# Optimization experiments

Hardware: AMD Instinct MI355X
Metric: run time of the kernel (lower is better)

The kernel has to match this reference:

```python
import jax, jax.numpy as jnp
import numpy as np

NUM_HEAD = 8
HEAD_DIM = 64
TEMPERATURE = 10000.0


def positional_encoding(L, D):
    # Mirrors get_positional_encoding: sin on even-indexed, cos on odd-indexed
    # columns of pos, interleaved via stack+reshape.
    embed = jnp.arange(L, dtype=jnp.float32)
    dim_t = jnp.arange(D, dtype=jnp.float32)
    dim_t = TEMPERATURE ** (2.0 * jnp.floor(dim_t / 2.0) / D)
    pos = embed[:, None] / dim_t                      # [L, D]
    pos = jnp.stack([jnp.sin(pos[:, 0::2]), jnp.cos(pos[:, 1::2])], axis=2)
    return pos.reshape(1, L, D)                       # [1, L, D]


def setup_inputs() -> dict:
    key = jax.random.key(0)
    ks = jax.random.split(key, 4)
    B, L, D = 8, 1024, 256
    HD = NUM_HEAD * HEAD_DIM                          # 512
    glorot = float(np.sqrt(2.0 / (D + HD)))
    return {
        "x": jax.random.normal(ks[0], (B, L, D), jnp.float32),
        "Wq": jax.random.normal(ks[1], (D, HD), jnp.float32) * glorot,
        "bq": jnp.zeros((NUM_HEAD,), jnp.float32),
        "Wk": jax.random.normal(ks[2], (D, HD), jnp.float32) * glorot,
        "bk": jnp.zeros((NUM_HEAD,), jnp.float32),
        "Wv": jax.random.normal(ks[3], (D, HD), jnp.float32) * glorot,
        "bv": jnp.zeros((NUM_HEAD,), jnp.float32),
    }


def reference(x, Wq, bq, Wk, bk, Wv, bv):
    B, L, D = x.shape
    pe = positional_encoding(L, D)
    qk_in = x + pe                                    # query/key get pos-enc, value does not
    # per-head bias broadcast over head_dim (tf.repeat(bias, head_dim))
    q = qk_in @ Wq + jnp.repeat(bq, HEAD_DIM)
    k = qk_in @ Wk + jnp.repeat(bk, HEAD_DIM)
    v = x @ Wv + jnp.repeat(bv, HEAD_DIM)
    split = lambda t: t.reshape(B, L, NUM_HEAD, HEAD_DIM)
    q, k, v = split(q), split(k), split(v)
    att = jnp.einsum('blhd,bmhd->bhlm', q, k) * (float(HEAD_DIM) ** -0.5)
    att = jax.nn.softmax(att, axis=-1)                # [B, H, L, L]
    out = jnp.einsum('bhlm,bmhd->blhd', att, v)       # [B, L, H, hd]
    return out.reshape(B, L, NUM_HEAD * HEAD_DIM)
```

## Files before the change

### kernel.cpp

```cpp
#include <hip/hip_runtime.h>
#include <hip/hip_bf16.h>

#define NB   8
#define NL   1024
#define ND   256
#define NH   8
#define NHD  64
#define NC   512
#define NTOK (NB*NL)

typedef __bf16 bf16x8v __attribute__((ext_vector_type(8)));
typedef float f32x4 __attribute__((ext_vector_type(4)));

__device__ __forceinline__ unsigned short f2bf(float f) {
  unsigned u = __float_as_uint(f);
  unsigned r = (u + 0x7fffu + ((u >> 16) & 1u)) >> 16;
  return (unsigned short)r;
}

__device__ __forceinline__ unsigned pack_bf16x2(float lo, float hi) {
  __hip_bfloat162 h2 = __float22bfloat162_rn(make_float2(lo, hi));
  union { __hip_bfloat162 h; unsigned u; } cvt;
  cvt.h = h2;
  return cvt.u;
}

__global__ __launch_bounds__(256) void gemm_qkv_fused_kernel(
    const float* __restrict__ x,
    const float* __restrict__ Wq, const float* __restrict__ Wk,
    const float* __restrict__ Wv,
    const float* __restrict__ bq, const float* __restrict__ bk,
    const float* __restrict__ bv,
    unsigned short* __restrict__ qg, unsigned short* __restrict__ kg,
    unsigned short* __restrict__ vg) {
  __shared__ unsigned short As[128 * 72];
  __shared__ unsigned short Bs[128 * 72];

  const int z = blockIdx.z;
  const float* Wsrc = (z == 0) ? Wq : (z == 1) ? Wk : Wv;
  const float* bias = (z == 0) ? bq : (z == 1) ? bk : bv;
  unsigned short* Out = (z == 0) ? qg : (z == 1) ? kg : vg;
  const float scale = (z == 0) ? 0.18033688011112042f : 1.0f;
  const bool addpe = (z < 2);

  const int nt = blockIdx.x;
  const int mt = blockIdx.y;
  const int tid = threadIdx.x;
  const int w = tid >> 6;
  const int wm = w >> 1, wn = w & 1;
  const int lane = tid & 63;
  const int lg = lane >> 4, lr = lane & 15;

  const int r0 = tid >> 3, c8 = tid & 7;
  unsigned short* Adst = As + r0 * 72 + 8 * ((c8 + 2 * (r0 & 7)) & 7);
  const float* xbase = x + (size_t)(mt * 128 + r0) * ND + c8 * 8;
  const int no = tid & 15, kp0 = tid >> 4;

  f32x4 acc[4][4] = {};

  for (int kb = 0; kb < 4; ++kb) {
    if (kb) __syncthreads();
    float i0 = 0.f, i1 = 0.f, i2 = 0.f, i3 = 0.f;
    if (addpe) {
      int dh = kb * 32 + c8 * 4;
      i0 = __expf(-0.07195578415606394f * (float)(dh));
      i1 = __expf(-0.07195578415606394f * (float)(dh + 1));
      i2 = __expf(-0.07195578415606394f * (float)(dh + 2));
      i3 = __expf(-0.07195578415606394f * (float)(dh + 3));
    }
#pragma unroll
    for (int i = 0; i < 4; ++i) {
      int row = r0 + 32 * i;
      f32x4 xa = *(const f32x4*)(xbase + (size_t)(32 * i) * ND + kb * 64);
      f32x4 xc = *(const f32x4*)(xbase + (size_t)(32 * i) * ND + kb * 64 + 4);
      unsigned p0, p1, p2, p3;
      if (addpe) {
        float l = (float)((mt * 128 + row) & (NL - 1));
        float a0 = l * i0, a1 = l * i1, a2 = l * i2, a3 = l * i3;
        p0 = pack_bf16x2(xa[0] + __sinf(a0), xa[1] + __cosf(a0));
        p1 = pack_bf16x2(xa[2] + __sinf(a1), xa[3] + __cosf(a1));
        p2 = pack_bf16x2(xc[0] + __sinf(a2), xc[1] + __cosf(a2));
        p3 = pack_bf16x2(xc[2] + __sinf(a3), xc[3] + __cosf(a3));
      } else {
        p0 = pack_bf16x2(xa[0], xa[1]);
        p1 = pack_bf16x2(xa[2], xa[3]);
        p2 = pack_bf16x2(xc[0], xc[1]);
        p3 = pack_bf16x2(xc[2], xc[3]);
      }
      int4 pv; pv.x = (int)p0; pv.y = (int)p1; pv.z = (int)p2; pv.w = (int)p3;
      *(int4*)(Adst + (size_t)(32 * i) * 72) = pv;
    }
#pragma unroll
    for (int u = 0; u < 2; ++u) {
      int kp = kp0 + 16 * u;
      int krow = kb * 64 + 2 * kp;
      const float* wr0 = Wsrc + (size_t)krow * NC + nt * 128 + no * 8;
      const float* wr1 = wr0 + NC;
      f32x4 w0a = *(const f32x4*)(wr0);
      f32x4 w0b = *(const f32x4*)(wr0 + 4);
      f32x4 w1a = *(const f32x4*)(wr1);
      f32x4 w1b = *(const f32x4*)(wr1 + 4);
#pragma unroll
      for (int e = 0; e < 8; ++e) {
        float lo = (e < 4) ? w0a[e] : w0b[e - 4];
        float hi = (e < 4) ? w1a[e] : w1b[e - 4];
        int n = no * 8 + e;
        *(unsigned*)(Bs + n * 72 + 8 * (((kp >> 2) + (no & 7)) & 7) +
                     (kp & 3) * 2) = pack_bf16x2(lo, hi);
      }
    }
    __syncthreads();

#pragma unroll
    for (int kk = 0; kk < 2; ++kk) {
      bf16x8v a[4], b[4];
#pragma unroll
      for (int mi = 0; mi < 4; ++mi) {
        int row = wm * 64 + mi * 16 + lr;
        a[mi] = *(const bf16x8v*)(As + row * 72 +
                                  8 * ((4 * kk + lg + 2 * (row & 7)) & 7));
      }
#pragma unroll
      for (int nj = 0; nj < 4; ++nj) {
        int n = wn * 64 + nj * 16 + lr;
        b[nj] = *(const bf16x8v*)(Bs + n * 72 +
                                  8 * ((4 * kk + lg + ((n >> 3) & 7)) & 7));
      }
#pragma unroll
      for (int mi = 0; mi < 4; ++mi)
#pragma unroll
        for (int nj = 0; nj < 4; ++nj)
          acc[mi][nj] = __builtin_amdgcn_mfma_f32_16x16x32_bf16(
              a[mi], b[nj], acc[mi][nj], 0, 0, 0);
    }
  }

  const float bval = bias[nt * 2 + wn];
  const int h = nt * 2 + wn;
#pragma unroll
  for (int mi = 0; mi < 4; ++mi) {
#pragma unroll
    for (int nj = 0; nj < 4; ++nj) {
#pragma unroll
      for (int j = 0; j < 4; ++j) {
        int r = mt * 128 + wm * 64 + mi * 16 + lg * 4 + j;
        int dd = nj * 16 + lr;
        int bb = r >> 10, lpos = r & (NL - 1);
        float val = (acc[mi][nj][j] + bval) * scale;
        if (z < 2)
          Out[((bb * NH + h) * NL + lpos) * NHD + dd] = f2bf(val);
        else
          Out[((bb * NH + h) * NHD + dd) * NL + lpos] = f2bf(val);
      }
    }
  }
}

__global__ __launch_bounds__(256) void attn_kernel(
    const unsigned short* __restrict__ Q,
    const unsigned short* __restrict__ K,
    const unsigned short* __restrict__ Vt,
    float* __restrict__ Out) {
  __shared__ unsigned short Ks[64 * 72];
  __shared__ unsigned short Vs[64 * 72];
  __shared__ unsigned short Ps[64 * 72];

  const int qt = blockIdx.x;
  const int bh = blockIdx.y;
  const int bb = bh >> 3, h = bh & 7;
  const int tid = threadIdx.x;
  const int w = tid >> 6;
  const int lane = tid & 63;
  const int lg = lane >> 4, lr = lane & 15;
  const int qrow0 = qt * 64 + w * 16;

  bf16x8v qf[2];
#pragma unroll
  for (int kk = 0; kk < 2; ++kk)
    qf[kk] = *(const bf16x8v*)(Q + ((size_t)bh * NL + qrow0 + lr) * NHD + kk * 32 + lg * 8);

  const int r0 = tid >> 3;
  const int c8 = tid & 7;
  const unsigned short* kp0 = K + (size_t)bh * NL * NHD + r0 * NHD + c8 * 8;
  const unsigned short* vp0 = Vt + ((size_t)bh * NHD + r0) * NL + c8 * 8;
  const int sw_st = 8 * ((c8 + 2 * (r0 & 7)) & 7);
  unsigned short* kdst = Ks + r0 * 72 + sw_st;
  unsigned short* vdst = Vs + r0 * 72 + sw_st;

  float m_ = -1e30f, lsum = 0.0f;
  f32x4 o[4] = {};
  int4 ka, kc, va, vc;

#define KVLOADS(kv)                                             \
  ka = *(const int4*)(kp0 + (kv) * 64 * NHD);                   \
  kc = *(const int4*)(kp0 + (kv) * 64 * NHD + 32 * NHD);        \
  va = *(const int4*)(vp0 + (kv) * 64);                         \
  vc = *(const int4*)(vp0 + (kv) * 64 + 32 * NL);

  KVLOADS(0)
  for (int kv = 0; kv < 16; ++kv) {
    if (kv) __syncthreads();
    *(int4*)(kdst)           = ka;
    *(int4*)(kdst + 32 * 72) = kc;
    *(int4*)(vdst)           = va;
    *(int4*)(vdst + 32 * 72) = vc;
    if (kv < 15) { KVLOADS(kv + 1) }
    __syncthreads();

    f32x4 s[4] = {};
    __builtin_amdgcn_s_setprio(1);
#pragma unroll
    for (int kk = 0; kk < 2; ++kk) {
#pragma unroll
      for (int nb = 0; nb < 4; ++nb) {
        int row = nb * 16 + lr;
        bf16x8v kf = *(const bf16x8v*)(Ks + row * 72 +
                                       8 * ((4 * kk + lg + 2 * (row & 7)) & 7));
        s[nb] = __builtin_amdgcn_mfma_f32_16x16x32_bf16(kf, qf[kk], s[nb], 0, 0, 0);
      }
    }
    __builtin_amdgcn_s_setprio(0);

    float tm;
    {
      float a0 = fmaxf(s[0][0], s[0][1]), a1 = fmaxf(s[0][2], s[0][3]);
      float a2 = fmaxf(s[1][0], s[1][1]), a3 = fmaxf(s[1][2], s[1][3]);
      float a4 = fmaxf(s[2][0], s[2][1]), a5 = fmaxf(s[2][2], s[2][3]);
      float a6 = fmaxf(s[3][0], s[3][1]), a7 = fmaxf(s[3][2], s[3][3]);
      float c0 = fmaxf(fmaxf(a0, a1), fmaxf(a2, a3));
      float c1 = fmaxf(fmaxf(a4, a5), fmaxf(a6, a7));
      tm = fmaxf(c0, c1);
    }
    tm = fmaxf(tm, __shfl_xor(tm, 16, 64));
    tm = fmaxf(tm, __shfl_xor(tm, 32, 64));
    if (__any(tm > m_ + 8.0f)) {
      float nm = fmaxf(m_, tm);
      float corr = exp2f(m_ - nm);
      m_ = nm;
      lsum *= corr;
#pragma unroll
      for (int db = 0; db < 4; ++db)
#pragma unroll
        for (int j = 0; j < 4; ++j) o[db][j] *= corr;
    }
#pragma unroll
    for (int nb = 0; nb < 4; ++nb)
#pragma unroll
      for (int j = 0; j < 4; ++j)
        s[nb][j] = exp2f(s[nb][j] - m_);
    float ts;
    {
      float a0 = s[0][0] + s[0][1], a1 = s[0][2] + s[0][3];
      float a2 = s[1][0] + s[1][1], a3 = s[1][2] + s[1][3];
      float a4 = s[2][0] + s[2][1], a5 = s[2][2] + s[2][3];
      float a6 = s[3][0] + s[3][1], a7 = s[3][2] + s[3][3];
      ts = ((a0 + a1) + (a2 + a3)) + ((a4 + a5) + (a6 + a7));
    }
    ts += __shfl_xor(ts, 16, 64);
    ts += __shfl_xor(ts, 32, 64);
    lsum += ts;

    {
      int prow = w * 16 + lr;
      unsigned short* pbase = Ps + prow * 72;
      int key = 2 * (lr & 7);
#pragma unroll
      for (int nb = 0; nb < 4; ++nb)
#pragma unroll
        for (int hh = 0; hh < 2; ++hh) {
          int slot = 2 * nb + (lg >> 1);
          *(unsigned*)(pbase + 8 * ((slot + key) & 7) + (lg & 1) * 4 + 2 * hh) =
              pack_bf16x2(s[nb][2 * hh], s[nb][2 * hh + 1]);
        }
    }

    __builtin_amdgcn_s_setprio(1);
#pragma unroll
    for (int kk = 0; kk < 2; ++kk) {
      int prow = w * 16 + lr;
      bf16x8v pf = *(const bf16x8v*)(Ps + prow * 72 +
                                     8 * ((4 * kk + lg + 2 * (lr & 7)) & 7));
#pragma unroll
      for (int db = 0; db < 4; ++db) {
        int row = db * 16 + lr;
        bf16x8v vf = *(const bf16x8v*)(Vs + row * 72 +
                                       8 * ((4 * kk + lg + 2 * (row & 7)) & 7));
        o[db] = __builtin_amdgcn_mfma_f32_16x16x32_bf16(vf, pf, o[db], 0, 0, 0);
      }
    }
    __builtin_amdgcn_s_setprio(0);
  }
#undef KVLOADS

  float inv = 1.0f / lsum;
  int q = qrow0 + lr;
#pragma unroll
  for (int db = 0; db < 4; ++db) {
    f32x4 ov;
#pragma unroll
    for (int j = 0; j < 4; ++j) ov[j] = o[db][j] * inv;
    *(f32x4*)(Out + (size_t)(bb * NL + q) * NC + h * NHD + db * 16 + lg * 4) = ov;
  }
}

extern "C" void kernel_launch(void* const* d_in, const int* in_sizes, int n_in,
                              void* d_out, int out_size, void* d_ws, size_t ws_size,
                              hipStream_t stream) {
  const float* x  = (const float*)d_in[0];
  const float* Wq = (const float*)d_in[1];
  const float* bq = (const float*)d_in[2];
  const float* Wk = (const float*)d_in[3];
  const float* bk = (const float*)d_in[4];
  const float* Wv = (const float*)d_in[5];
  const float* bv = (const float*)d_in[6];
  float* out = (float*)d_out;

  unsigned short* qg = (unsigned short*)d_ws;
  unsigned short* kg = qg + (size_t)NB * NH * NL * NHD;
  unsigned short* vg = kg + (size_t)NB * NH * NL * NHD;

  gemm_qkv_fused_kernel<<<dim3(4, 64, 3), 256, 0, stream>>>(
      x, Wq, Wk, Wv, bq, bk, bv, qg, kg, vg);

  attn_kernel<<<dim3(16, 64), 256, 0, stream>>>(qg, kg, vg, out);
}
```

Baseline: 134.5 us.

## Stage V transpose through LDS and drop XOR swizzle in attention tiles

For the V projection, the GEMM epilogue now writes the tile transposed into shared memory and then stores 128-bit contiguous rows to the transposed V output. Before, each thread issued strided 2-byte scattered stores. The attention kernel removes the XOR swizzle on the K, V and P shared tiles and relies on the 72-element row padding alone to avoid bank conflicts, which simplifies address arithmetic. The tradeoff is two extra barriers in the V epilogue and possibly more LDS bank conflicts in attention without the swizzle.

```diff
diff --git a/kernel.cpp b/kernel.cpp
--- a/kernel.cpp
+++ b/kernel.cpp
@@ -33,8 +33,9 @@
     const float* __restrict__ bv,
     unsigned short* __restrict__ qg, unsigned short* __restrict__ kg,
     unsigned short* __restrict__ vg) {
-  __shared__ unsigned short As[128 * 72];
-  __shared__ unsigned short Bs[128 * 72];
+  __shared__ unsigned short smem[2 * 128 * 72];
+  unsigned short* As = smem;
+  unsigned short* Bs = smem + 128 * 72;
 
   const int z = blockIdx.z;
   const float* Wsrc = (z == 0) ? Wq : (z == 1) ? Wk : Wv;
@@ -137,22 +138,48 @@
 
   const float bval = bias[nt * 2 + wn];
   const int h = nt * 2 + wn;
-#pragma unroll
-  for (int mi = 0; mi < 4; ++mi) {
-#pragma unroll
-    for (int nj = 0; nj < 4; ++nj) {
-#pragma unroll
-      for (int j = 0; j < 4; ++j) {
-        int r = mt * 128 + wm * 64 + mi * 16 + lg * 4 + j;
-        int dd = nj * 16 + lr;
-        int bb = r >> 10, lpos = r & (NL - 1);
-        float val = (acc[mi][nj][j] + bval) * scale;
-        if (z < 2)
+  if (z < 2) {
+#pragma unroll
+    for (int mi = 0; mi < 4; ++mi) {
+#pragma unroll
+      for (int nj = 0; nj < 4; ++nj) {
+#pragma unroll
+        for (int j = 0; j < 4; ++j) {
+          int r = mt * 128 + wm * 64 + mi * 16 + lg * 4 + j;
+          int dd = nj * 16 + lr;
+          int bb = r >> 10, lpos = r & (NL - 1);
+          float val = (acc[mi][nj][j] + bval) * scale;
           Out[((bb * NH + h) * NL + lpos) * NHD + dd] = f2bf(val);
-        else
-          Out[((bb * NH + h) * NHD + dd) * NL + lpos] = f2bf(val);
-      }
-    }
+        }
+      }
+    }
+  } else {
+    __syncthreads();
+    unsigned short* Ts = smem;
+#pragma unroll
+    for (int mi = 0; mi < 4; ++mi)
+#pragma unroll
+      for (int nj = 0; nj < 4; ++nj)
+#pragma unroll
+        for (int jp = 0; jp < 2; ++jp) {
+          int c = wn * 64 + nj * 16 + lr;
+          int r = wm * 64 + mi * 16 + lg * 4 + jp * 2;
+          *(unsigned*)(Ts + c * 136 + r) =
+              pack_bf16x2(acc[mi][nj][jp * 2] + bval,
+                          acc[mi][nj][jp * 2 + 1] + bval);
+        }
+    __syncthreads();
+    int row = tid >> 1, half = tid & 1;
+    int hh = nt * 2 + (row >> 6);
+    int ddl = row & 63;
+    int bb2 = (mt * 128) >> 10;
+    int lpos0 = (mt * 128) & (NL - 1);
+    unsigned short* dst =
+        Out + ((size_t)(bb2 * NH + hh) * NHD + ddl) * NL + lpos0 + half * 64;
+    const unsigned short* src = Ts + row * 136 + half * 64;
+#pragma unroll
+    for (int i = 0; i < 8; ++i)
+      *(int4*)(dst + i * 8) = *(const int4*)(src + i * 8);
   }
 }
 
@@ -180,12 +207,11 @@
     qf[kk] = *(const bf16x8v*)(Q + ((size_t)bh * NL + qrow0 + lr) * NHD + kk * 32 + lg * 8);
 
   const int r0 = tid >> 3;
-  const int c8 = tid & 7;
-  const unsigned short* kp0 = K + (size_t)bh * NL * NHD + r0 * NHD + c8 * 8;
-  const unsigned short* vp0 = Vt + ((size_t)bh * NHD + r0) * NL + c8 * 8;
-  const int sw_st = 8 * ((c8 + 2 * (r0 & 7)) & 7);
-  unsigned short* kdst = Ks + r0 * 72 + sw_st;
-  unsigned short* vdst = Vs + r0 * 72 + sw_st;
+  const int c8o = (tid & 7) * 8;
+  const unsigned short* kp0 = K + (size_t)bh * NL * NHD + r0 * NHD + c8o;
+  const unsigned short* vp0 = Vt + ((size_t)bh * NHD + r0) * NL + c8o;
+  unsigned short* kdst = Ks + r0 * 72 + c8o;
+  unsigned short* vdst = Vs + r0 * 72 + c8o;
 
   float m_ = -1e30f, lsum = 0.0f;
   f32x4 o[4] = {};
@@ -213,9 +239,7 @@
     for (int kk = 0; kk < 2; ++kk) {
 #pragma unroll
       for (int nb = 0; nb < 4; ++nb) {
-        int row = nb * 16 + lr;
-        bf16x8v kf = *(const bf16x8v*)(Ks + row * 72 +
-                                       8 * ((4 * kk + lg + 2 * (row & 7)) & 7));
+        bf16x8v kf = *(const bf16x8v*)(Ks + (nb * 16 + lr) * 72 + kk * 32 + lg * 8);
         s[nb] = __builtin_amdgcn_mfma_f32_16x16x32_bf16(kf, qf[kk], s[nb], 0, 0, 0);
       }
     }
@@ -260,31 +284,20 @@
     ts += __shfl_xor(ts, 32, 64);
     lsum += ts;
 
-    {
-      int prow = w * 16 + lr;
-      unsigned short* pbase = Ps + prow * 72;
-      int key = 2 * (lr & 7);
-#pragma unroll
-      for (int nb = 0; nb < 4; ++nb)
-#pragma unroll
-        for (int hh = 0; hh < 2; ++hh) {
-          int slot = 2 * nb + (lg >> 1);
-          *(unsigned*)(pbase + 8 * ((slot + key) & 7) + (lg & 1) * 4 + 2 * hh) =
-              pack_bf16x2(s[nb][2 * hh], s[nb][2 * hh + 1]);
-        }
-    }
+#pragma unroll
+    for (int nb = 0; nb < 4; ++nb)
+#pragma unroll
+      for (int hh = 0; hh < 2; ++hh)
+        *(unsigned*)(Ps + (w * 16 + lr) * 72 + nb * 16 + lg * 4 + 2 * hh) =
+            pack_bf16x2(s[nb][2 * hh], s[nb][2 * hh + 1]);
 
     __builtin_amdgcn_s_setprio(1);
 #pragma unroll
     for (int kk = 0; kk < 2; ++kk) {
-      int prow = w * 16 + lr;
-      bf16x8v pf = *(const bf16x8v*)(Ps + prow * 72 +
-                                     8 * ((4 * kk + lg + 2 * (lr & 7)) & 7));
+      bf16x8v pf = *(const bf16x8v*)(Ps + (w * 16 + lr) * 72 + kk * 32 + lg * 8);
 #pragma unroll
       for (int db = 0; db < 4; ++db) {
-        int row = db * 16 + lr;
-        bf16x8v vf = *(const bf16x8v*)(Vs + row * 72 +
-                                       8 * ((4 * kk + lg + 2 * (row & 7)) & 7));
+        bf16x8v vf = *(const bf16x8v*)(Vs + (db * 16 + lr) * 72 + kk * 32 + lg * 8);
         o[db] = __builtin_amdgcn_mfma_f32_16x16x32_bf16(vf, pf, o[db], 0, 0, 0);
       }
     }
```

New measurement: 141.4 us. 5.1% more time.
